# Kernel tuning notes

Hardware: AMD Instinct MI355X
Metric: run time of the kernel (lower is better)

The kernel has to match this reference:

```python
import jax, jax.numpy as jnp
import numpy as np

NUM_NODES = 4096


def _dense_adjs(edge_index, edge_values, n):
    # edge_index: [J, 2, E] int, edge_values: [J, E] float -> [J, n, n]
    # scatter-add == torch_sparse.coalesce (duplicate edges are summed)
    def one(ei, ev):
        return jnp.zeros((n, n), ev.dtype).at[ei[0], ei[1]].add(ev)
    return jax.vmap(one)(edge_index, edge_values)


def setup_inputs() -> dict:
    key = jax.random.key(0)
    k1, k2, k3, k4 = jax.random.split(key, 4)
    J, E, C, N = 5, 150000, 2, NUM_NODES
    edge_index = jax.random.randint(k1, (J, 2, E), 0, N)
    edge_values = jax.random.uniform(k2, (J, E), dtype=jnp.float32)
    w1 = jax.random.normal(k3, (C, J), dtype=jnp.float32) * 0.01
    w2 = jax.random.normal(k4, (C, J), dtype=jnp.float32) * 0.01
    return {"edge_index": edge_index, "edge_values": edge_values, "w1": w1, "w2": w2}


def reference(edge_index, edge_values, w1, w2):
    n = NUM_NODES
    # GTConv: softmax over edge types, weighted sum of per-type adjacencies
    D = _dense_adjs(edge_index, edge_values, n)          # [J, n, n]
    f1 = jax.nn.softmax(w1, axis=1)                      # [C, J]
    f2 = jax.nn.softmax(w2, axis=1)                      # [C, J]
    A1 = jnp.einsum('cj,jmn->cmn', f1, D)                # conv1 output per channel
    A2 = jnp.einsum('cj,jmn->cmn', f2, D)                # conv2 output per channel
    # spspmm per channel == dense matmul of the (zero-padded) sparse matrices
    H = jnp.einsum('cmk,ckn->cmn', A1, A2)               # [C, n, n]
    return (H, f1, f2)
```

## Files before the change

### kernel.cpp

```cpp
#include <hip/hip_runtime.h>
#include <hip/hip_bf16.h>
#include <stdint.h>

#define JT 5
#define NE 150000
#define NC 2
#define NDIM 4096
#define KDIM 4096
#define NNZ (JT * NE)
constexpr size_t MAT = (size_t)NDIM * NDIM;
constexpr size_t HN  = (size_t)NC * MAT;

typedef __bf16 bf16x8 __attribute__((ext_vector_type(8)));
typedef float  f32x4  __attribute__((ext_vector_type(4)));

__global__ void softmax_k(const float* __restrict__ w1, const float* __restrict__ w2,
                          float* __restrict__ fbuf, float* __restrict__ out_tail) {
    int t = threadIdx.x;
    if (t < 2 * NC) {
        const float* w = (t < NC) ? w1 : w2;
        int c = t % NC;
        float v[JT];
        float mx = -1e30f;
        for (int j = 0; j < JT; ++j) { v[j] = w[c * JT + j]; mx = fmaxf(mx, v[j]); }
        float s = 0.f;
        for (int j = 0; j < JT; ++j) { v[j] = expf(v[j] - mx); s += v[j]; }
        float inv = 1.0f / s;
        for (int j = 0; j < JT; ++j) {
            float f = v[j] * inv;
            fbuf[t * JT + j] = f;
            out_tail[t * JT + j] = f;
        }
    }
}

__device__ __forceinline__ void pkadd2(__bf16* p, float lo, float hi) {
    uint16_t a = __builtin_bit_cast(uint16_t, (__bf16)lo);
    uint16_t b = __builtin_bit_cast(uint16_t, (__bf16)hi);
    uint32_t pk = ((uint32_t)b << 16) | a;
    asm volatile("global_atomic_pk_add_bf16 %0, %1, off"
                 :: "v"((uint64_t)(uintptr_t)p), "v"(pk) : "memory");
}

__global__ void scatter2_k(const int* __restrict__ ei, const float* __restrict__ ev,
                           const float* __restrict__ fbuf, __bf16* __restrict__ Xi) {
    int idx = blockIdx.x * blockDim.x + threadIdx.x;
    if (idx >= NNZ) return;
    int j = idx / NE;
    int e = idx - j * NE;
    int r = ei[(size_t)j * 2 * NE + e];
    int c = ei[(size_t)j * 2 * NE + NE + e];
    float v = ev[idx];
    size_t cell = ((size_t)r * NDIM + c) * 4;
    pkadd2(Xi + cell,     fbuf[j]          * v, fbuf[JT + j]     * v);
    pkadd2(Xi + cell + 2, fbuf[2 * JT + j] * v, fbuf[3 * JT + j] * v);
}

__device__ __forceinline__ uint4 gather8(const ushort (*s)[65], int rr, int e8) {
    uint4 v;
    v.x = (uint32_t)s[rr][e8 + 0] | ((uint32_t)s[rr][e8 + 1] << 16);
    v.y = (uint32_t)s[rr][e8 + 2] | ((uint32_t)s[rr][e8 + 3] << 16);
    v.z = (uint32_t)s[rr][e8 + 4] | ((uint32_t)s[rr][e8 + 5] << 16);
    v.w = (uint32_t)s[rr][e8 + 6] | ((uint32_t)s[rr][e8 + 7] << 16);
    return v;
}

__global__ __launch_bounds__(256) void repack_k(const ushort4* __restrict__ Xi,
                                                __bf16* __restrict__ A1,
                                                __bf16* __restrict__ A2T) {
    __shared__ ushort s10[64][65];
    __shared__ ushort s11[64][65];
    __shared__ ushort s20[64][65];
    __shared__ ushort s21[64][65];
    const int r0 = blockIdx.y * 64, c0 = blockIdx.x * 64;
    const int t = threadIdx.x;

#pragma unroll
    for (int it = 0; it < 16; ++it) {
        int li = t + 256 * it;
        int rr = li >> 6, cc = li & 63;
        ushort4 v = Xi[(size_t)(r0 + rr) * NDIM + (c0 + cc)];
        s10[rr][cc] = v.x; s11[rr][cc] = v.y;
        s20[cc][rr] = v.z; s21[cc][rr] = v.w;
    }
    __syncthreads();

#pragma unroll
    for (int a = 0; a < 2; ++a) {
        int w = t + 256 * a;
        int rr = w >> 3, e8 = (w & 7) << 3;
        *(uint4*)(A1 +        (size_t)(r0 + rr) * NDIM + c0 + e8) = gather8(s10, rr, e8);
        *(uint4*)(A1 + MAT +  (size_t)(r0 + rr) * NDIM + c0 + e8) = gather8(s11, rr, e8);
        *(uint4*)(A2T +       (size_t)(c0 + rr) * NDIM + r0 + e8) = gather8(s20, rr, e8);
        *(uint4*)(A2T + MAT + (size_t)(c0 + rr) * NDIM + r0 + e8) = gather8(s21, rr, e8);
    }
}

#define BM 256
#define BN 256
#define BK 64
#define NT (KDIM / BK)
#define TILE_E (BM * BK)

__device__ __forceinline__ void gl_lds16(const __bf16* g, __bf16* l) {
    __builtin_amdgcn_global_load_lds(
        (const __attribute__((address_space(1))) void*)(uintptr_t)g,
        (__attribute__((address_space(3))) void*)l, 16, 0, 0);
}

#define PHASE(MH, KS, READB, ...) do {                                            \
    _Pragma("unroll")                                                             \
    for (int i = 0; i < 4; ++i)                                                   \
        af[i] = *(const bf16x8*)(ldsAc +                                          \
            ((((rA + ((MH)*4 + i) * 16) * 128) + (KS)*64 + kb) ^ swz));           \
    if (READB) {                                                                  \
        _Pragma("unroll")                                                         \
        for (int n = 0; n < 4; ++n)                                               \
            bfr[n] = *(const bf16x8*)(ldsBc +                                     \
                ((((rB + n * 16) * 128) + (KS)*64 + kb) ^ swz));                  \
    }                                                                             \
    __VA_ARGS__;                                                                  \
    __builtin_amdgcn_s_barrier();                                                 \
    asm volatile("s_waitcnt lgkmcnt(0)" ::: "memory");                            \
    __builtin_amdgcn_s_setprio(1);                                                \
    _Pragma("unroll")                                                             \
    for (int i = 0; i < 4; ++i)                                                   \
        _Pragma("unroll")                                                         \
        for (int n = 0; n < 4; ++n)                                               \
            acc[(MH)*4 + i][n] = __builtin_amdgcn_mfma_f32_16x16x32_bf16(         \
                af[i], bfr[n], acc[(MH)*4 + i][n], 0, 0, 0);                      \
    __builtin_amdgcn_s_setprio(0);                                                \
    __builtin_amdgcn_s_barrier();                                                 \
} while (0)

__global__ __launch_bounds__(512, 2) void gemm_k(const __bf16* __restrict__ A,
                                                 const __bf16* __restrict__ B,
                                                 float* __restrict__ C) {
    __shared__ __align__(16) __bf16 sm[4 * TILE_E];

    const int u    = threadIdx.x;
    const int lane = u & 63;
    const int wv   = u >> 6;
    const int wm   = wv >> 2;
    const int wn   = wv & 3;
    const size_t matoff = (size_t)blockIdx.z * MAT;
    const size_t brow   = (size_t)blockIdx.y * BM;
    const size_t bcol   = (size_t)blockIdx.x * BN;

    const int srow = u >> 3;
    const int kc   = (u & 7) ^ (srow & 7);
    const __bf16* Abase = A + matoff + (brow + srow) * KDIM + kc * 8;
    const __bf16* Bbase = B + matoff + (bcol + srow) * KDIM + kc * 8;

    char* const smb = (char*)sm;
    auto issueA = [&](int unit, int tt) {
        const __bf16* src = Abase + (size_t)unit * 64 * KDIM + (size_t)tt * BK;
        __bf16* dst = (__bf16*)(smb + (tt & 1) * 65536 + unit * 8192 + wv * 1024);
        gl_lds16(src, dst);
    };
    auto issueB = [&](int unit, int tt) {
        const __bf16* src = Bbase + (size_t)unit * 64 * KDIM + (size_t)tt * BK;
        __bf16* dst = (__bf16*)(smb + (tt & 1) * 65536 + 32768 + unit * 8192 + wv * 1024);
        gl_lds16(src, dst);
    };

    const int rA  = wm * 128 + (lane & 15);
    const int rB  = wn * 64  + (lane & 15);
    const int kb  = (lane >> 4) * 16;
    const int swz = (lane & 7) << 4;

    f32x4 acc[8][4];
#pragma unroll
    for (int m = 0; m < 8; ++m)
#pragma unroll
        for (int n = 0; n < 4; ++n) acc[m][n] = (f32x4){0.f, 0.f, 0.f, 0.f};

    bf16x8 af[4], bfr[4];

#pragma unroll
    for (int i = 0; i < 4; ++i) issueA(i, 0);
#pragma unroll
    for (int i = 0; i < 4; ++i) issueB(i, 0);

    for (int t = 0; t < NT; ++t) {
        const char* ldsAc = smb + (t & 1) * 65536;
        const char* ldsBc = ldsAc + 32768;
        const int nxt = t + 1;
        const bool hasNext = nxt < NT;

        if (hasNext) {
            issueA(0, nxt); issueA(1, nxt);
            asm volatile("s_waitcnt vmcnt(2)" ::: "memory");
        } else {
            asm volatile("s_waitcnt vmcnt(0)" ::: "memory");
        }
        __builtin_amdgcn_s_barrier();
        asm volatile("" ::: "memory");

        PHASE(0, 0, true,  if (hasNext) { issueA(2, nxt); issueA(3, nxt);
                                          issueB(0, nxt); issueB(1, nxt); });
        PHASE(1, 0, false, if (hasNext) { issueB(2, nxt); issueB(3, nxt); });
        PHASE(0, 1, true,  );
        PHASE(1, 1, false, );
    }

    float* Cc = C + matoff;
#pragma unroll
    for (int m = 0; m < 8; ++m) {
        int orow0 = (int)brow + wm * 128 + m * 16 + (lane >> 4) * 4;
#pragma unroll
        for (int n = 0; n < 4; ++n) {
            int ocol = (int)bcol + wn * 64 + n * 16 + (lane & 15);
            float* p = Cc + (size_t)orow0 * NDIM + ocol;
#pragma unroll
            for (int jj = 0; jj < 4; ++jj) p[(size_t)jj * NDIM] = acc[m][n][jj];
        }
    }
}

extern "C" void kernel_launch(void* const* d_in, const int* in_sizes, int n_in,
                              void* d_out, int out_size, void* d_ws, size_t ws_size,
                              hipStream_t stream) {
    const int*   ei = (const int*)d_in[0];
    const float* ev = (const float*)d_in[1];
    const float* w1 = (const float*)d_in[2];
    const float* w2 = (const float*)d_in[3];
    float* out = (float*)d_out;

    char* ws = (char*)d_ws;
    __bf16* A1b  = (__bf16*)ws;
    __bf16* A2b  = (__bf16*)(ws + HN * sizeof(__bf16));
    float*  fbuf = (float*)(ws + 2 * HN * sizeof(__bf16));
    size_t needed = 2 * HN * sizeof(__bf16) + 32 * sizeof(float);
    if (ws_size < needed) return;

    __bf16* Xi = (__bf16*)d_out;

    softmax_k<<<dim3(1), dim3(64), 0, stream>>>(w1, w2, fbuf, out + HN);

    hipMemsetAsync(Xi, 0, HN * sizeof(float), stream);

    const int nb = (NNZ + 255) / 256;
    scatter2_k<<<dim3(nb), dim3(256), 0, stream>>>(ei, ev, fbuf, Xi);

    repack_k<<<dim3(64, 64), dim3(256), 0, stream>>>((const ushort4*)Xi, A1b, A2b);

    gemm_k<<<dim3(NDIM / BN, NDIM / BM, NC), dim3(512), 0, stream>>>(A1b, A2b, out);
}
```

Before: 358.0 us.

## Restructure GEMM into quadrant-wise stages with finer-grained load/compute interleave

Splits the 256x256 block tile into four 128x128 quadrants, each computed by all 8 waves with a 64x32 per-wave subtile, and reorders the main loop so each quadrant's MFMA batch follows a staged half-tile global-to-LDS load for the next K step. Per-wave A/B fragments now cover both K halves in one read, barriers are gated on vmcnt counts, and the last iteration is peeled out. The aim is to overlap global loads with MFMA work more evenly and cut barrier count per K step. The risks are more LDS fragment reads per MFMA, which may raise LDS pressure, and possible races in the double-buffer reuse timing.

```diff
diff --git a/kernel.cpp b/kernel.cpp
--- a/kernel.cpp
+++ b/kernel.cpp
@@ -100,7 +100,6 @@
 #define BN 256
 #define BK 64
 #define NT (KDIM / BK)
-#define TILE_E (BM * BK)
 
 __device__ __forceinline__ void gl_lds16(const __bf16* g, __bf16* l) {
     __builtin_amdgcn_global_load_lds(
@@ -108,114 +107,146 @@
         (__attribute__((address_space(3))) void*)l, 16, 0, 0);
 }
 
-#define PHASE(MH, KS, READB, ...) do {                                            \
+#define READA(AH) do {                                                            \
     _Pragma("unroll")                                                             \
     for (int i = 0; i < 4; ++i)                                                   \
-        af[i] = *(const bf16x8*)(ldsAc +                                          \
-            ((((rA + ((MH)*4 + i) * 16) * 128) + (KS)*64 + kb) ^ swz));           \
-    if (READB) {                                                                  \
         _Pragma("unroll")                                                         \
-        for (int n = 0; n < 4; ++n)                                               \
-            bfr[n] = *(const bf16x8*)(ldsBc +                                     \
-                ((((rB + n * 16) * 128) + (KS)*64 + kb) ^ swz));                  \
-    }                                                                             \
-    __VA_ARGS__;                                                                  \
-    __builtin_amdgcn_s_barrier();                                                 \
+        for (int ks = 0; ks < 2; ++ks)                                            \
+            af[i][ks] = *(const bf16x8*)(ldsAc + (AH) * 16384 +                   \
+                ((((rAl + i * 16) * 128) + ks * 64 + kb) ^ swz));                 \
+} while (0)
+
+#define READB(BH) do {                                                            \
+    _Pragma("unroll")                                                             \
+    for (int n = 0; n < 2; ++n)                                                   \
+        _Pragma("unroll")                                                         \
+        for (int ks = 0; ks < 2; ++ks)                                            \
+            bf_[n][ks] = *(const bf16x8*)(ldsBc + (BH) * 16384 +                  \
+                ((((rBl + n * 16) * 128) + ks * 64 + kb) ^ swz));                 \
+} while (0)
+
+#define MFMA16(AH, BH) do {                                                       \
     asm volatile("s_waitcnt lgkmcnt(0)" ::: "memory");                            \
     __builtin_amdgcn_s_setprio(1);                                                \
     _Pragma("unroll")                                                             \
     for (int i = 0; i < 4; ++i)                                                   \
         _Pragma("unroll")                                                         \
-        for (int n = 0; n < 4; ++n)                                               \
-            acc[(MH)*4 + i][n] = __builtin_amdgcn_mfma_f32_16x16x32_bf16(         \
-                af[i], bfr[n], acc[(MH)*4 + i][n], 0, 0, 0);                      \
+        for (int n = 0; n < 2; ++n)                                               \
+            _Pragma("unroll")                                                     \
+            for (int ks = 0; ks < 2; ++ks)                                        \
+                acc[AH][BH][i][n] = __builtin_amdgcn_mfma_f32_16x16x32_bf16(      \
+                    af[i][ks], bf_[n][ks], acc[AH][BH][i][n], 0, 0, 0);           \
     __builtin_amdgcn_s_setprio(0);                                                \
+} while (0)
+
+#define GATE_BAR(N) do {                                                          \
+    asm volatile("s_waitcnt vmcnt(" #N ")" ::: "memory");                         \
     __builtin_amdgcn_s_barrier();                                                 \
+    asm volatile("" ::: "memory");                                                \
 } while (0)
 
 __global__ __launch_bounds__(512, 2) void gemm_k(const __bf16* __restrict__ A,
                                                  const __bf16* __restrict__ B,
                                                  float* __restrict__ C) {
-    __shared__ __align__(16) __bf16 sm[4 * TILE_E];
+    __shared__ __align__(16) __bf16 sm[65536];
 
     const int u    = threadIdx.x;
     const int lane = u & 63;
     const int wv   = u >> 6;
-    const int wm   = wv >> 2;
-    const int wn   = wv & 3;
+    const int wr   = (wv >> 2) * 64;
+    const int wc   = (wv & 3) * 32;
     const size_t matoff = (size_t)blockIdx.z * MAT;
     const size_t brow   = (size_t)blockIdx.y * BM;
     const size_t bcol   = (size_t)blockIdx.x * BN;
 
     const int srow = u >> 3;
     const int kc   = (u & 7) ^ (srow & 7);
-    const __bf16* Abase = A + matoff + (brow + srow) * KDIM + kc * 8;
-    const __bf16* Bbase = B + matoff + (bcol + srow) * KDIM + kc * 8;
-
+    const __bf16* Ab = A + matoff + (brow + srow) * KDIM + kc * 8;
+    const __bf16* Bb = B + matoff + (bcol + srow) * KDIM + kc * 8;
     char* const smb = (char*)sm;
-    auto issueA = [&](int unit, int tt) {
-        const __bf16* src = Abase + (size_t)unit * 64 * KDIM + (size_t)tt * BK;
-        __bf16* dst = (__bf16*)(smb + (tt & 1) * 65536 + unit * 8192 + wv * 1024);
-        gl_lds16(src, dst);
+
+    auto stage = [&](int mat, int h, int tt) {
+        const __bf16* base = mat ? Bb : Ab;
+#pragma unroll
+        for (int unit = 0; unit < 2; ++unit) {
+            const __bf16* src = base + (size_t)(h * 128 + unit * 64) * KDIM + (size_t)tt * BK;
+            __bf16* dst = (__bf16*)(smb + (tt & 1) * 65536 + mat * 32768 +
+                                    h * 16384 + unit * 8192 + wv * 1024);
+            gl_lds16(src, dst);
+        }
     };
-    auto issueB = [&](int unit, int tt) {
-        const __bf16* src = Bbase + (size_t)unit * 64 * KDIM + (size_t)tt * BK;
-        __bf16* dst = (__bf16*)(smb + (tt & 1) * 65536 + 32768 + unit * 8192 + wv * 1024);
-        gl_lds16(src, dst);
-    };
-
-    const int rA  = wm * 128 + (lane & 15);
-    const int rB  = wn * 64  + (lane & 15);
+
+    const int rAl = wr + (lane & 15);
+    const int rBl = wc + (lane & 15);
     const int kb  = (lane >> 4) * 16;
     const int swz = (lane & 7) << 4;
 
-    f32x4 acc[8][4];
-#pragma unroll
-    for (int m = 0; m < 8; ++m)
-#pragma unroll
-        for (int n = 0; n < 4; ++n) acc[m][n] = (f32x4){0.f, 0.f, 0.f, 0.f};
-
-    bf16x8 af[4], bfr[4];
-
-#pragma unroll
-    for (int i = 0; i < 4; ++i) issueA(i, 0);
-#pragma unroll
-    for (int i = 0; i < 4; ++i) issueB(i, 0);
-
-    for (int t = 0; t < NT; ++t) {
+    f32x4 acc[2][2][4][2];
+#pragma unroll
+    for (int a = 0; a < 2; ++a)
+#pragma unroll
+        for (int b = 0; b < 2; ++b)
+#pragma unroll
+            for (int i = 0; i < 4; ++i)
+#pragma unroll
+                for (int n = 0; n < 2; ++n) acc[a][b][i][n] = (f32x4){0.f, 0.f, 0.f, 0.f};
+
+    bf16x8 af[4][2], bf_[2][2];
+
+    stage(0, 0, 0); stage(1, 0, 0); stage(1, 1, 0); stage(0, 1, 0);
+
+    for (int t = 0; t < NT - 1; ++t) {
         const char* ldsAc = smb + (t & 1) * 65536;
         const char* ldsBc = ldsAc + 32768;
         const int nxt = t + 1;
-        const bool hasNext = nxt < NT;
-
-        if (hasNext) {
-            issueA(0, nxt); issueA(1, nxt);
-            asm volatile("s_waitcnt vmcnt(2)" ::: "memory");
-        } else {
-            asm volatile("s_waitcnt vmcnt(0)" ::: "memory");
-        }
-        __builtin_amdgcn_s_barrier();
-        asm volatile("" ::: "memory");
-
-        PHASE(0, 0, true,  if (hasNext) { issueA(2, nxt); issueA(3, nxt);
-                                          issueB(0, nxt); issueB(1, nxt); });
-        PHASE(1, 0, false, if (hasNext) { issueB(2, nxt); issueB(3, nxt); });
-        PHASE(0, 1, true,  );
-        PHASE(1, 1, false, );
+        GATE_BAR(4);
+        stage(0, 0, nxt);
+        READA(0); READB(0);
+        MFMA16(0, 0);
+        GATE_BAR(4);
+        stage(1, 0, nxt);
+        READB(1);
+        MFMA16(0, 1);
+        GATE_BAR(4);
+        stage(1, 1, nxt);
+        READA(1);
+        MFMA16(1, 1);
+        stage(0, 1, nxt);
+        READB(0);
+        MFMA16(1, 0);
+    }
+    {
+        const char* ldsAc = smb + ((NT - 1) & 1) * 65536;
+        const char* ldsBc = ldsAc + 32768;
+        GATE_BAR(4);
+        READA(0); READB(0);
+        MFMA16(0, 0);
+        GATE_BAR(2);
+        READB(1);
+        MFMA16(0, 1);
+        GATE_BAR(0);
+        READA(1);
+        MFMA16(1, 1);
+        READB(0);
+        MFMA16(1, 0);
     }
 
     float* Cc = C + matoff;
 #pragma unroll
-    for (int m = 0; m < 8; ++m) {
-        int orow0 = (int)brow + wm * 128 + m * 16 + (lane >> 4) * 4;
-#pragma unroll
-        for (int n = 0; n < 4; ++n) {
-            int ocol = (int)bcol + wn * 64 + n * 16 + (lane & 15);
-            float* p = Cc + (size_t)orow0 * NDIM + ocol;
-#pragma unroll
-            for (int jj = 0; jj < 4; ++jj) p[(size_t)jj * NDIM] = acc[m][n][jj];
-        }
-    }
+    for (int a = 0; a < 2; ++a)
+#pragma unroll
+        for (int b = 0; b < 2; ++b)
+#pragma unroll
+            for (int i = 0; i < 4; ++i) {
+                int orow0 = (int)brow + a * 128 + wr + i * 16 + (lane >> 4) * 4;
+#pragma unroll
+                for (int n = 0; n < 2; ++n) {
+                    int ocol = (int)bcol + b * 128 + wc + n * 16 + (lane & 15);
+                    float* p = Cc + (size_t)orow0 * NDIM + ocol;
+#pragma unroll
+                    for (int jj = 0; jj < 4; ++jj) p[(size_t)jj * NDIM] = acc[a][b][i][n][jj];
+                }
+            }
 }
 
 extern "C" void kernel_launch(void* const* d_in, const int* in_sizes, int n_in,
```

After: 338.5 us. 1.06x faster.
